# Kernel tuning notes

Measured on AMD Instinct MI355X. Metric: run time of the kernel, lower is better.

The kernel has to match this reference:

```python
import jax, jax.numpy as jnp
import numpy as np

LN_EPS = 1e-5
NUM_BIAS_TYPES = 10


def _layernorm(h, g, b):
    mu = jnp.mean(h, axis=-1, keepdims=True)
    var = jnp.var(h, axis=-1, keepdims=True)
    return (h - mu) * jax.lax.rsqrt(var + LN_EPS) * g + b


def _quat_mul(q, p):
    # Hamilton product q*p; q broadcastable to p, last dim = 4 (w,x,y,z)
    w1, x1, y1, z1 = q[..., 0], q[..., 1], q[..., 2], q[..., 3]
    w2, x2, y2, z2 = p[..., 0], p[..., 1], p[..., 2], p[..., 3]
    return jnp.stack([
        w1 * w2 - x1 * x2 - y1 * y2 - z1 * z2,
        w1 * x2 + x1 * w2 + y1 * z2 - z1 * y2,
        w1 * y2 - x1 * z2 + y1 * w2 + z1 * x2,
        w1 * z2 + x1 * y2 - y1 * x2 + z1 * w2,
    ], axis=-1)


def setup_inputs() -> dict:
    key = jax.random.key(0)
    ks = jax.random.split(key, 8)
    B, T, E = 8, 4096, 1024
    H = E // 2
    s1 = 1.0 / np.sqrt(E)
    s2 = 1.0 / np.sqrt(E)
    s3 = 1.0 / np.sqrt(H)
    return {
        "x": jax.random.normal(ks[0], (B, T, E), jnp.float32),
        "W1": jax.random.uniform(ks[1], (E, E), jnp.float32, -s1, s1),
        "b1": jnp.zeros((E,), jnp.float32),
        "ln_g": jnp.ones((E,), jnp.float32),
        "ln_b": jnp.zeros((E,), jnp.float32),
        "W2": jax.random.uniform(ks[2], (H, E), jnp.float32, -s2, s2),
        "b2": jnp.zeros((H,), jnp.float32),
        "W3": jax.random.uniform(ks[3], (NUM_BIAS_TYPES, H), jnp.float32, -s3, s3),
        "b3": jnp.zeros((NUM_BIAS_TYPES,), jnp.float32),
        "quats": jax.random.normal(ks[4], (NUM_BIAS_TYPES, 4), jnp.float32) * 0.1,
        "threshold": jnp.array([0.6], jnp.float32),
    }


def reference(x, W1, b1, ln_g, ln_b, W2, b2, W3, b3, quats, threshold):
    B, T, E = x.shape
    # bias detector MLP (exact-erf GELU, as torch nn.GELU default)
    h = jnp.einsum('bte,fe->btf', x, W1) + b1
    h = jax.nn.gelu(_layernorm(h, ln_g, ln_b), approximate=False)
    h = jax.nn.gelu(jnp.einsum('bte,fe->btf', h, W2) + b2, approximate=False)
    bias_scores = jax.nn.sigmoid(jnp.einsum('bth,nh->btn', h, W3) + b3)  # [B,T,10]

    thr = threshold[0]
    xq = x.reshape(B, T, E // 4, 4)
    # sequentially apply each bias type's quaternion correction (compounding, as original)
    for i in range(NUM_BIAS_TYPES):
        mask = bias_scores[:, :, i] > thr  # [B,T]
        rotated = _quat_mul(quats[i], xq)
        xq = jnp.where(mask[:, :, None, None], rotated, xq)
    return xq.reshape(B, T, E)
```

## Files before the change

### kernel.cpp

```cpp
#include <hip/hip_runtime.h>
#include <hip/hip_bf16.h>
#include <math.h>


#define M_TOK (8 * 4096)
#define E_DIM 1024
#define H_DIM 512
#define NBIAS 10
#define NXCD 8

typedef unsigned short ushort_t;
typedef unsigned int u32;
typedef __attribute__((ext_vector_type(8))) short bf16x8;
typedef __attribute__((ext_vector_type(4))) float f32x4;

__device__ __forceinline__ float gelu_erf(float t) {
    return 0.5f * t * (1.0f + erff(t * 0.70710678118654752440f));
}
__device__ __forceinline__ float bf2f(ushort_t h) {
    return __uint_as_float((u32)h << 16);
}
__device__ __forceinline__ ushort_t f2bf(float f) {
    u32 u = __float_as_uint(f);
    u32 r = 0x7fffu + ((u >> 16) & 1u);
    return (ushort_t)((u + r) >> 16);
}

__global__ __launch_bounds__(256) void conv_split_kernel(
    const float* __restrict__ src, ushort_t* __restrict__ hi,
    ushort_t* __restrict__ lo, int n4) {
    for (int i = blockIdx.x * 256 + threadIdx.x; i < n4; i += gridDim.x * 256) {
        float4 v = ((const float4*)src)[i];
        ushort4 h, l;
        h.x = f2bf(v.x); l.x = f2bf(v.x - bf2f(h.x));
        h.y = f2bf(v.y); l.y = f2bf(v.y - bf2f(h.y));
        h.z = f2bf(v.z); l.z = f2bf(v.z - bf2f(h.z));
        h.w = f2bf(v.w); l.w = f2bf(v.w - bf2f(h.w));
        ((ushort4*)hi)[i] = h;
        ((ushort4*)lo)[i] = l;
    }
}

template <int SPLIT_OUT>
__global__ __launch_bounds__(256) void gemm_mfma_split(
    const ushort_t* __restrict__ Ahi, const ushort_t* __restrict__ Alo,
    const ushort_t* __restrict__ Bhi, const ushort_t* __restrict__ Blo,
    const float* __restrict__ bias,
    ushort_t* __restrict__ Chi, ushort_t* __restrict__ Clo,
    float* __restrict__ Cf, int N, int K) {
    __shared__ ushort_t lds[4][128 * 32];

    const int tid = threadIdx.x;
    const int w = tid >> 6, lane = tid & 63;

    const int nwg = gridDim.x * gridDim.y;
    const int lin = blockIdx.y * gridDim.x + blockIdx.x;
    const int q = nwg / NXCD, rr = nwg % NXCD;
    const int xcd = lin % NXCD, pos = lin / NXCD;
    const int newlin = (xcd < rr ? xcd * (q + 1) : rr * (q + 1) + (xcd - rr) * q) + pos;
    const int bm = (newlin / gridDim.x) * 128;
    const int bn = (newlin % gridDim.x) * 128;

    const int wr = w >> 1, wc = w & 1;

    const ushort_t* gsrc = (w == 0) ? Ahi : (w == 1) ? Alo : (w == 2) ? Bhi : Blo;
    const int grow0 = (w < 2) ? bm : bn;
    const int cswz = (((lane & 3) - ((lane >> 3) & 3)) & 3) * 8;
    const ushort_t* gbase = gsrc + (size_t)(grow0 + (lane >> 2)) * K + cswz;

    f32x4 acc[4][4] = {};

    const int arow = wr * 64 + (lane & 15);
    const int brow = wc * 64 + (lane & 15);
    const int kgrp = ((((lane >> 4) + ((lane & 15) >> 1)) & 3)) * 8;

    for (int k0 = 0; k0 < K; k0 += 32) {
        __syncthreads();
#pragma unroll
        for (int s = 0; s < 8; ++s) {
            __builtin_amdgcn_global_load_lds(
                (const __attribute__((address_space(1))) u32*)(const void*)(gbase + (size_t)(s * 16) * K + k0),
                (__attribute__((address_space(3))) u32*)(void*)(&lds[w][s * 16 * 32]),
                16, 0, 0);
        }
        __syncthreads();

        bf16x8 a[2][4], b[2][4];
#pragma unroll
        for (int m = 0; m < 4; ++m) {
            a[0][m] = *(const bf16x8*)&lds[0][(arow + m * 16) * 32 + kgrp];
            a[1][m] = *(const bf16x8*)&lds[1][(arow + m * 16) * 32 + kgrp];
        }
#pragma unroll
        for (int n = 0; n < 4; ++n) {
            b[0][n] = *(const bf16x8*)&lds[2][(brow + n * 16) * 32 + kgrp];
            b[1][n] = *(const bf16x8*)&lds[3][(brow + n * 16) * 32 + kgrp];
        }
#pragma unroll
        for (int m = 0; m < 4; ++m)
#pragma unroll
            for (int n = 0; n < 4; ++n) {
                acc[m][n] = __builtin_amdgcn_mfma_f32_16x16x32_bf16(a[0][m], b[0][n], acc[m][n], 0, 0, 0);
                acc[m][n] = __builtin_amdgcn_mfma_f32_16x16x32_bf16(a[0][m], b[1][n], acc[m][n], 0, 0, 0);
                acc[m][n] = __builtin_amdgcn_mfma_f32_16x16x32_bf16(a[1][m], b[0][n], acc[m][n], 0, 0, 0);
            }
    }

    const int crow0 = bm + wr * 64 + (lane >> 4) * 4;
    const int ccol0 = bn + wc * 64;
    const int csub = lane & 15;
#pragma unroll
    for (int m = 0; m < 4; ++m)
#pragma unroll
        for (int n = 0; n < 4; ++n) {
            const int col = ccol0 + n * 16 + csub;
            const float bv = bias[col];
#pragma unroll
            for (int r = 0; r < 4; ++r) {
                const size_t idx = (size_t)(crow0 + m * 16 + r) * N + col;
                const float v = acc[m][n][r] + bv;
                if (SPLIT_OUT) {
                    const ushort_t h = f2bf(v);
                    Chi[idx] = h;
                    Clo[idx] = f2bf(v - bf2f(h));
                } else {
                    Cf[idx] = gelu_erf(v);
                }
            }
        }
}

__global__ __launch_bounds__(256) void ln_gelu_split_kernel(
    ushort_t* __restrict__ hhi, ushort_t* __restrict__ hlo,
    const float* __restrict__ gamma, const float* __restrict__ beta) {
    __shared__ float sbuf[8];
    const int tid = threadIdx.x;
    const size_t base = (size_t)blockIdx.x * E_DIM + tid * 4;
    const ushort4 vh = *(const ushort4*)(hhi + base);
    const ushort4 vl = *(const ushort4*)(hlo + base);
    float f0 = bf2f(vh.x) + bf2f(vl.x);
    float f1 = bf2f(vh.y) + bf2f(vl.y);
    float f2 = bf2f(vh.z) + bf2f(vl.z);
    float f3 = bf2f(vh.w) + bf2f(vl.w);

    float s = f0 + f1 + f2 + f3;
#pragma unroll
    for (int off = 1; off < 64; off <<= 1) s += __shfl_xor(s, off);
    if ((tid & 63) == 0) sbuf[tid >> 6] = s;
    __syncthreads();
    const float mean = (sbuf[0] + sbuf[1] + sbuf[2] + sbuf[3]) * (1.0f / E_DIM);

    const float d0 = f0 - mean, d1 = f1 - mean, d2 = f2 - mean, d3 = f3 - mean;
    float s2 = d0 * d0 + d1 * d1 + d2 * d2 + d3 * d3;
#pragma unroll
    for (int off = 1; off < 64; off <<= 1) s2 += __shfl_xor(s2, off);
    if ((tid & 63) == 0) sbuf[4 + (tid >> 6)] = s2;
    __syncthreads();
    const float var = (sbuf[4] + sbuf[5] + sbuf[6] + sbuf[7]) * (1.0f / E_DIM);
    const float rstd = 1.0f / sqrtf(var + 1e-5f);

    const float4 gm = ((const float4*)gamma)[tid];
    const float4 bt = ((const float4*)beta)[tid];
    float o0 = gelu_erf(d0 * rstd * gm.x + bt.x);
    float o1 = gelu_erf(d1 * rstd * gm.y + bt.y);
    float o2 = gelu_erf(d2 * rstd * gm.z + bt.z);
    float o3 = gelu_erf(d3 * rstd * gm.w + bt.w);

    ushort4 oh, ol;
    oh.x = f2bf(o0); ol.x = f2bf(o0 - bf2f(oh.x));
    oh.y = f2bf(o1); ol.y = f2bf(o1 - bf2f(oh.y));
    oh.z = f2bf(o2); ol.z = f2bf(o2 - bf2f(oh.z));
    oh.w = f2bf(o3); ol.w = f2bf(o3 - bf2f(oh.w));
    *(ushort4*)(hhi + base) = oh;
    *(ushort4*)(hlo + base) = ol;
}

__global__ __launch_bounds__(256) void score_rotate_kernel(
    const float* __restrict__ g, const float* __restrict__ W3,
    const float* __restrict__ b3, const float* __restrict__ quats,
    const float* __restrict__ thr_p, const float* __restrict__ x,
    float* __restrict__ out) {
    const int lane = threadIdx.x & 63;
    const int wid = threadIdx.x >> 6;
    const int token = blockIdx.x * 4 + wid;

    const float4* grow = (const float4*)(g + (size_t)token * H_DIM);
    const float4 g0 = grow[lane * 2 + 0];
    const float4 g1 = grow[lane * 2 + 1];

    float dots[NBIAS];
#pragma unroll
    for (int n = 0; n < NBIAS; ++n) {
        const float4* wr = (const float4*)(W3 + n * H_DIM);
        const float4 w0 = wr[lane * 2 + 0];
        const float4 w1 = wr[lane * 2 + 1];
        float d = g0.x * w0.x + g0.y * w0.y + g0.z * w0.z + g0.w * w0.w;
        d += g1.x * w1.x + g1.y * w1.y + g1.z * w1.z + g1.w * w1.w;
        dots[n] = d;
    }
#pragma unroll
    for (int off = 1; off < 64; off <<= 1)
#pragma unroll
        for (int n = 0; n < NBIAS; ++n) dots[n] += __shfl_xor(dots[n], off);

    const float thr = thr_p[0];
    float qw = 1.0f, qx = 0.0f, qy = 0.0f, qz = 0.0f;
#pragma unroll
    for (int n = 0; n < NBIAS; ++n) {
        const float z = dots[n] + b3[n];
        const float s = 1.0f / (1.0f + expf(-z));
        if (s > thr) {
            const float w1 = quats[n * 4 + 0], x1 = quats[n * 4 + 1];
            const float y1 = quats[n * 4 + 2], z1 = quats[n * 4 + 3];
            const float nw = w1 * qw - x1 * qx - y1 * qy - z1 * qz;
            const float nx = w1 * qx + x1 * qw + y1 * qz - z1 * qy;
            const float ny = w1 * qy - x1 * qz + y1 * qw + z1 * qx;
            const float nz = w1 * qz + x1 * qy - y1 * qx + z1 * qw;
            qw = nw; qx = nx; qy = ny; qz = nz;
        }
    }

    const float4* xr = (const float4*)(x + (size_t)token * E_DIM);
    float4* orow = (float4*)(out + (size_t)token * E_DIM);
#pragma unroll
    for (int j = 0; j < 4; ++j) {
        const float4 p = xr[lane * 4 + j];
        float4 r;
        r.x = qw * p.x - qx * p.y - qy * p.z - qz * p.w;
        r.y = qw * p.y + qx * p.x + qy * p.w - qz * p.z;
        r.z = qw * p.z - qx * p.w + qy * p.x + qz * p.y;
        r.w = qw * p.w + qx * p.z - qy * p.y + qz * p.x;
        orow[lane * 4 + j] = r;
    }
}

extern "C" void kernel_launch(void* const* d_in, const int* in_sizes, int n_in,
                              void* d_out, int out_size, void* d_ws, size_t ws_size,
                              hipStream_t stream) {
    const float* x     = (const float*)d_in[0];
    const float* W1    = (const float*)d_in[1];
    const float* b1    = (const float*)d_in[2];
    const float* ln_g  = (const float*)d_in[3];
    const float* ln_b  = (const float*)d_in[4];
    const float* W2    = (const float*)d_in[5];
    const float* b2    = (const float*)d_in[6];
    const float* W3    = (const float*)d_in[7];
    const float* b3    = (const float*)d_in[8];
    const float* quats = (const float*)d_in[9];
    const float* thr   = (const float*)d_in[10];
    float* out = (float*)d_out;

    char* p = (char*)d_ws;
    ushort_t* W1hi = (ushort_t*)p; p += (size_t)E_DIM * E_DIM * 2;
    ushort_t* W1lo = (ushort_t*)p; p += (size_t)E_DIM * E_DIM * 2;
    ushort_t* W2hi = (ushort_t*)p; p += (size_t)H_DIM * E_DIM * 2;
    ushort_t* W2lo = (ushort_t*)p; p += (size_t)H_DIM * E_DIM * 2;
    const size_t fixed = (size_t)(p - (char*)d_ws);

    int Mc = M_TOK;
    while (Mc > 128) {
        const size_t need = fixed + (size_t)Mc * (E_DIM * 2 * 2  + E_DIM * 2 * 2  + H_DIM * 4 );
        if (need <= ws_size) break;
        Mc >>= 1;
    }
    ushort_t* xhi = (ushort_t*)p; p += (size_t)Mc * E_DIM * 2;
    ushort_t* xlo = (ushort_t*)p; p += (size_t)Mc * E_DIM * 2;
    ushort_t* hhi = (ushort_t*)p; p += (size_t)Mc * E_DIM * 2;
    ushort_t* hlo = (ushort_t*)p; p += (size_t)Mc * E_DIM * 2;
    float*    gb  = (float*)p;

    dim3 blk(256);
    {
        int n4 = E_DIM * E_DIM / 4;
        conv_split_kernel<<<dim3(min(2048, (n4 + 255) / 256)), blk, 0, stream>>>(W1, W1hi, W1lo, n4);
        n4 = H_DIM * E_DIM / 4;
        conv_split_kernel<<<dim3(min(2048, (n4 + 255) / 256)), blk, 0, stream>>>(W2, W2hi, W2lo, n4);
    }

    for (int r0 = 0; r0 < M_TOK; r0 += Mc) {
        const float* xc = x + (size_t)r0 * E_DIM;
        const int n4 = Mc * E_DIM / 4;
        conv_split_kernel<<<dim3(min(2048, (n4 + 255) / 256)), blk, 0, stream>>>(xc, xhi, xlo, n4);
        gemm_mfma_split<1><<<dim3(E_DIM / 128, Mc / 128), blk, 0, stream>>>(
            xhi, xlo, W1hi, W1lo, b1, hhi, hlo, nullptr, E_DIM, E_DIM);
        ln_gelu_split_kernel<<<dim3(Mc), blk, 0, stream>>>(hhi, hlo, ln_g, ln_b);
        gemm_mfma_split<0><<<dim3(H_DIM / 128, Mc / 128), blk, 0, stream>>>(
            hhi, hlo, W2hi, W2lo, b2, nullptr, nullptr, gb, H_DIM, E_DIM);
        score_rotate_kernel<<<dim3(Mc / 4), blk, 0, stream>>>(
            gb, W3, b3, quats, thr, xc, out + (size_t)r0 * E_DIM);
    }
}
```

Baseline: 763.4 us.

## Rewrite split-bf16 GEMM as 256x256 tile, 8-wave, 4-stage pipelined kernel

Replaces the 128x128 four-wave GEMM with a 256x256 tile and 512 threads, each wave holding an 8x4 block of accumulators. The three split-precision products (hi*hi, hi*lo, lo*hi) are flattened into 96 sequential k-phases over a 4-deep LDS ring, with async global_load_lds prefetch three phases ahead. Partial vmcnt waits, one barrier per phase, and s_setprio around the MFMA bursts replace the two full syncthreads per k-step. K is hardcoded to 1024, and larger tiles mean fewer workgroups, which may leave CUs underused for the N=512 GEMM.

New measurement: 693.5 us. -9.2%, faster.

```diff
diff --git a/kernel.cpp b/kernel.cpp
--- a/kernel.cpp
+++ b/kernel.cpp
@@ -42,75 +42,114 @@
 }
 
 template <int SPLIT_OUT>
-__global__ __launch_bounds__(256) void gemm_mfma_split(
+__global__ __launch_bounds__(512, 2) void gemm8p(
     const ushort_t* __restrict__ Ahi, const ushort_t* __restrict__ Alo,
     const ushort_t* __restrict__ Bhi, const ushort_t* __restrict__ Blo,
     const float* __restrict__ bias,
     ushort_t* __restrict__ Chi, ushort_t* __restrict__ Clo,
-    float* __restrict__ Cf, int N, int K) {
-    __shared__ ushort_t lds[4][128 * 32];
+    float* __restrict__ Cf, int N) {
+    constexpr int K = 1024;
+    constexpr int NT = 96;
+    __shared__ ushort_t lds[65536];
 
     const int tid = threadIdx.x;
     const int w = tid >> 6, lane = tid & 63;
+    const int wm = w >> 2, wn = w & 3;
 
     const int nwg = gridDim.x * gridDim.y;
     const int lin = blockIdx.y * gridDim.x + blockIdx.x;
     const int q = nwg / NXCD, rr = nwg % NXCD;
     const int xcd = lin % NXCD, pos = lin / NXCD;
     const int newlin = (xcd < rr ? xcd * (q + 1) : rr * (q + 1) + (xcd - rr) * q) + pos;
-    const int bm = (newlin / gridDim.x) * 128;
-    const int bn = (newlin % gridDim.x) * 128;
-
-    const int wr = w >> 1, wc = w & 1;
-
-    const ushort_t* gsrc = (w == 0) ? Ahi : (w == 1) ? Alo : (w == 2) ? Bhi : Blo;
-    const int grow0 = (w < 2) ? bm : bn;
+    const int bm = (newlin / gridDim.x) * 256;
+    const int bn = (newlin % gridDim.x) * 256;
+
     const int cswz = (((lane & 3) - ((lane >> 3) & 3)) & 3) * 8;
-    const ushort_t* gbase = gsrc + (size_t)(grow0 + (lane >> 2)) * K + cswz;
-
-    f32x4 acc[4][4] = {};
-
-    const int arow = wr * 64 + (lane & 15);
-    const int brow = wc * 64 + (lane & 15);
-    const int kgrp = ((((lane >> 4) + ((lane & 15) >> 1)) & 3)) * 8;
-
-    for (int k0 = 0; k0 < K; k0 += 32) {
-        __syncthreads();
-#pragma unroll
-        for (int s = 0; s < 8; ++s) {
-            __builtin_amdgcn_global_load_lds(
-                (const __attribute__((address_space(1))) u32*)(const void*)(gbase + (size_t)(s * 16) * K + k0),
-                (__attribute__((address_space(3))) u32*)(void*)(&lds[w][s * 16 * 32]),
-                16, 0, 0);
-        }
-        __syncthreads();
-
-        bf16x8 a[2][4], b[2][4];
-#pragma unroll
-        for (int m = 0; m < 4; ++m) {
-            a[0][m] = *(const bf16x8*)&lds[0][(arow + m * 16) * 32 + kgrp];
-            a[1][m] = *(const bf16x8*)&lds[1][(arow + m * 16) * 32 + kgrp];
-        }
-#pragma unroll
-        for (int n = 0; n < 4; ++n) {
-            b[0][n] = *(const bf16x8*)&lds[2][(brow + n * 16) * 32 + kgrp];
-            b[1][n] = *(const bf16x8*)&lds[3][(brow + n * 16) * 32 + kgrp];
-        }
+    const size_t aoff0 = (size_t)(bm + w * 16 + (lane >> 2)) * K + cswz;
+    const size_t aoff1 = (size_t)(bm + 128 + w * 16 + (lane >> 2)) * K + cswz;
+    const size_t boff0 = (size_t)(bn + w * 16 + (lane >> 2)) * K + cswz;
+    const size_t boff1 = (size_t)(bn + 128 + w * 16 + (lane >> 2)) * K + cswz;
+    const u32 ldw = w * 512;
+
+    const int pr = (((lane >> 4) + (((lane & 15) >> 1) & 3)) & 3) * 8;
+    const u32 arow_base = (u32)((wm * 128 + (lane & 15)) * 32) + pr;
+    const u32 brow_base = (u32)((wn * 64 + (lane & 15)) * 32) + pr;
+
+    f32x4 acc[8][4] = {};
+
+#define STAGE_A(pt) do { \
+    const int sg_ = (pt) >> 5; \
+    const size_t kk_ = (size_t)(((pt) & 31) * 32); \
+    const ushort_t* As_ = (sg_ == 2) ? Alo : Ahi; \
+    const u32 db_ = ((u32)((pt) & 3)) * 16384 + ldw; \
+    __builtin_amdgcn_global_load_lds( \
+        (const __attribute__((address_space(1))) u32*)(const void*)(As_ + aoff0 + kk_), \
+        (__attribute__((address_space(3))) u32*)(void*)(&lds[db_]), 16, 0, 0); \
+    __builtin_amdgcn_global_load_lds( \
+        (const __attribute__((address_space(1))) u32*)(const void*)(As_ + aoff1 + kk_), \
+        (__attribute__((address_space(3))) u32*)(void*)(&lds[db_ + 4096]), 16, 0, 0); \
+} while (0)
+
+#define STAGE_B(pt) do { \
+    const int sg_ = (pt) >> 5; \
+    const size_t kk_ = (size_t)(((pt) & 31) * 32); \
+    const ushort_t* Bs_ = (sg_ == 1) ? Blo : Bhi; \
+    const u32 db_ = ((u32)((pt) & 3)) * 16384 + 8192 + ldw; \
+    __builtin_amdgcn_global_load_lds( \
+        (const __attribute__((address_space(1))) u32*)(const void*)(Bs_ + boff0 + kk_), \
+        (__attribute__((address_space(3))) u32*)(void*)(&lds[db_]), 16, 0, 0); \
+    __builtin_amdgcn_global_load_lds( \
+        (const __attribute__((address_space(1))) u32*)(const void*)(Bs_ + boff1 + kk_), \
+        (__attribute__((address_space(3))) u32*)(void*)(&lds[db_ + 4096]), 16, 0, 0); \
+} while (0)
+
+    STAGE_A(0); STAGE_B(0);
+    STAGE_A(1); STAGE_B(1);
+    STAGE_A(2); STAGE_B(2);
+    asm volatile("s_waitcnt vmcnt(8)" ::: "memory");
+    __builtin_amdgcn_s_barrier();
+    asm volatile("" ::: "memory");
+
+    for (int t = 0; t < NT; ++t) {
+        const u32 ab = ((u32)(t & 3)) * 16384;
+        const u32 bb = ab + 8192;
+        bf16x8 bf[4], af[4];
+#pragma unroll
+        for (int n = 0; n < 4; ++n) bf[n] = *(const bf16x8*)&lds[bb + brow_base + n * 512];
+#pragma unroll
+        for (int m = 0; m < 4; ++m) af[m] = *(const bf16x8*)&lds[ab + arow_base + m * 512];
+        if (t + 3 < NT) STAGE_A(t + 3);
+        __builtin_amdgcn_s_setprio(1);
 #pragma unroll
         for (int m = 0; m < 4; ++m)
 #pragma unroll
-            for (int n = 0; n < 4; ++n) {
-                acc[m][n] = __builtin_amdgcn_mfma_f32_16x16x32_bf16(a[0][m], b[0][n], acc[m][n], 0, 0, 0);
-                acc[m][n] = __builtin_amdgcn_mfma_f32_16x16x32_bf16(a[0][m], b[1][n], acc[m][n], 0, 0, 0);
-                acc[m][n] = __builtin_amdgcn_mfma_f32_16x16x32_bf16(a[1][m], b[0][n], acc[m][n], 0, 0, 0);
-            }
-    }
-
-    const int crow0 = bm + wr * 64 + (lane >> 4) * 4;
-    const int ccol0 = bn + wc * 64;
+            for (int n = 0; n < 4; ++n)
+                acc[m][n] = __builtin_amdgcn_mfma_f32_16x16x32_bf16(af[m], bf[n], acc[m][n], 0, 0, 0);
+        __builtin_amdgcn_s_setprio(0);
+#pragma unroll
+        for (int m = 0; m < 4; ++m) af[m] = *(const bf16x8*)&lds[ab + arow_base + (m + 4) * 512];
+        if (t + 3 < NT) STAGE_B(t + 3);
+        __builtin_amdgcn_s_setprio(1);
+#pragma unroll
+        for (int m = 0; m < 4; ++m)
+#pragma unroll
+            for (int n = 0; n < 4; ++n)
+                acc[m + 4][n] = __builtin_amdgcn_mfma_f32_16x16x32_bf16(af[m], bf[n], acc[m + 4][n], 0, 0, 0);
+        __builtin_amdgcn_s_setprio(0);
+        if (t + 3 < NT)      asm volatile("s_waitcnt vmcnt(8)" ::: "memory");
+        else if (t + 2 < NT) asm volatile("s_waitcnt vmcnt(4)" ::: "memory");
+        else                 asm volatile("s_waitcnt vmcnt(0)" ::: "memory");
+        __builtin_amdgcn_s_barrier();
+        asm volatile("" ::: "memory");
+    }
+#undef STAGE_A
+#undef STAGE_B
+
+    const int crow0 = bm + wm * 128 + (lane >> 4) * 4;
+    const int ccol0 = bn + wn * 64;
     const int csub = lane & 15;
 #pragma unroll
-    for (int m = 0; m < 4; ++m)
+    for (int m = 0; m < 8; ++m)
 #pragma unroll
         for (int n = 0; n < 4; ++n) {
             const int col = ccol0 + n * 16 + csub;
@@ -258,7 +297,7 @@
     const size_t fixed = (size_t)(p - (char*)d_ws);
 
     int Mc = M_TOK;
-    while (Mc > 128) {
+    while (Mc > 256) {
         const size_t need = fixed + (size_t)Mc * (E_DIM * 2 * 2  + E_DIM * 2 * 2  + H_DIM * 4 );
         if (need <= ws_size) break;
         Mc >>= 1;
@@ -281,11 +320,11 @@
         const float* xc = x + (size_t)r0 * E_DIM;
         const int n4 = Mc * E_DIM / 4;
         conv_split_kernel<<<dim3(min(2048, (n4 + 255) / 256)), blk, 0, stream>>>(xc, xhi, xlo, n4);
-        gemm_mfma_split<1><<<dim3(E_DIM / 128, Mc / 128), blk, 0, stream>>>(
-            xhi, xlo, W1hi, W1lo, b1, hhi, hlo, nullptr, E_DIM, E_DIM);
+        gemm8p<1><<<dim3(E_DIM / 256, Mc / 256), dim3(512), 0, stream>>>(
+            xhi, xlo, W1hi, W1lo, b1, hhi, hlo, nullptr, E_DIM);
         ln_gelu_split_kernel<<<dim3(Mc), blk, 0, stream>>>(hhi, hlo, ln_g, ln_b);
-        gemm_mfma_split<0><<<dim3(H_DIM / 128, Mc / 128), blk, 0, stream>>>(
-            hhi, hlo, W2hi, W2lo, b2, nullptr, nullptr, gb, H_DIM, E_DIM);
+        gemm8p<0><<<dim3(H_DIM / 256, Mc / 256), dim3(512), 0, stream>>>(
+            hhi, hlo, W2hi, W2lo, b2, nullptr, nullptr, gb, H_DIM);
         score_rotate_kernel<<<dim3(Mc / 4), blk, 0, stream>>>(
             gb, W3, b3, quats, thr, xc, out + (size_t)r0 * E_DIM);
     }
```
